# Performance work log

Measured on AMD Instinct MI355X. Metric: run time of the kernel, lower is better.

The kernel has to match this reference:

```python
import jax, jax.numpy as jnp
import numpy as np

B = 256      # graphs per batch
N = 512      # nodes per graph (uniform)
D = 256      # in_channels
DEG = 16     # avg degree for synthetic edges
RATIO = 0.5
K = int(np.ceil(RATIO * N))  # nodes kept per graph = 256


def setup_inputs() -> dict:
    key = jax.random.key(0)
    k1, k2, k3 = jax.random.split(key, 3)
    x = jax.random.normal(k1, (B * N, D), dtype=jnp.float32)
    weight = jax.random.normal(k2, (D,), dtype=jnp.float32)  # TopKPooling score weight
    edge_index = jax.random.randint(k3, (2, B * N * DEG), 0, B * N, dtype=jnp.int64)
    batch = jnp.repeat(jnp.arange(B, dtype=jnp.int64), N)  # graph id per node
    return {"x": x, "weight": weight, "edge_index": edge_index, "batch": batch}


def reference(x, weight, edge_index, batch):
    # PyG TopKPooling: score = tanh((x . w) / ||w||); keep per-graph top-k nodes;
    # pooled features = x[perm] * score[perm]; then global_mean_pool over each graph.
    # Edge filtering/reindexing in TopKPooling does not affect this module's output
    # (forward returns only the mean-pooled node features), so edge_index/batch are
    # consumed but the filtered edges are dead w.r.t. the returned value.
    del edge_index, batch
    score = jnp.tanh((x @ weight) / jnp.linalg.norm(weight))          # [B*N]
    score_bn = score.reshape(B, N)                                     # segment-wise view
    top_s, top_i = jax.lax.top_k(score_bn, K)                          # [B,K] per-graph topk
    x_bn = x.reshape(B, N, D)
    x_sel = jnp.take_along_axis(x_bn, top_i[:, :, None], axis=1)       # [B,K,D] gather
    pooled = x_sel * top_s[:, :, None]                                 # gate by tanh score
    return pooled.mean(axis=1)                                         # global_mean_pool -> [B,D]
```

## Files before the change

kernel.cpp:

```cpp
#include <hip/hip_runtime.h>
#include <math.h>
#include <stdint.h>

#define BG 256
#define NN 512
#define DD 256
#define KK 256
#define WAVES 16

__device__ __forceinline__ uint32_t flip_f32(float f) {
    const uint32_t u = __float_as_uint(f);
    return (u & 0x80000000u) ? ~u : (u | 0x80000000u);
}

__global__ __launch_bounds__(1024) void topk_pool_fused(const float* __restrict__ x,
                                                        const float* __restrict__ w,
                                                        float* __restrict__ out) {
    __shared__ float s[NN];
    __shared__ int   lidx[KK];
    __shared__ float lval[KK];
    __shared__ float red[WAVES][DD];

    const int b    = blockIdx.x;
    const int wv   = threadIdx.x >> 6;
    const int lane = threadIdx.x & 63;

    const float4 w4 = *reinterpret_cast<const float4*>(w + lane * 4);
    float nw = fmaf(w4.x, w4.x, fmaf(w4.y, w4.y, fmaf(w4.z, w4.z, w4.w * w4.w)));
#pragma unroll
    for (int off = 32; off >= 1; off >>= 1) nw += __shfl_xor(nw, off);
    const float inv_nrm = rsqrtf(nw);

    const float* xg = x + (size_t)b * NN * DD;

    {
        const float* xp = xg + (size_t)(wv * 32) * DD + lane * 4;
#pragma unroll
        for (int r0 = 0; r0 < 32; r0 += 8) {
            float d[8];
#pragma unroll
            for (int j = 0; j < 8; ++j) {
                const float4 a = *reinterpret_cast<const float4*>(xp + (size_t)(r0 + j) * DD);
                d[j] = fmaf(a.x, w4.x, fmaf(a.y, w4.y, fmaf(a.z, w4.z, a.w * w4.w)));
            }
#pragma unroll
            for (int off = 32; off >= 1; off >>= 1) {
#pragma unroll
                for (int j = 0; j < 8; ++j) d[j] += __shfl_xor(d[j], off);
            }
#pragma unroll
            for (int j = 0; j < 8; ++j) d[j] = tanhf(d[j] * inv_nrm);
            if (lane == 0) {
                float4 o0 = {d[0], d[1], d[2], d[3]};
                float4 o1 = {d[4], d[5], d[6], d[7]};
                *reinterpret_cast<float4*>(&s[wv * 32 + r0])     = o0;
                *reinterpret_cast<float4*>(&s[wv * 32 + r0 + 4]) = o1;
            }
        }
    }
    __syncthreads();

    if (wv == 0) {
        float sv[8];
        const float4 a0 = *reinterpret_cast<const float4*>(&s[lane * 8]);
        const float4 a1 = *reinterpret_cast<const float4*>(&s[lane * 8 + 4]);
        sv[0] = a0.x; sv[1] = a0.y; sv[2] = a0.z; sv[3] = a0.w;
        sv[4] = a1.x; sv[5] = a1.y; sv[6] = a1.z; sv[7] = a1.w;

        uint32_t u[8];
#pragma unroll
        for (int j = 0; j < 8; ++j) u[j] = flip_f32(sv[j]);

        uint32_t p = 0u;
        for (int bit = 31; bit >= 0; --bit) {
            const uint32_t cand = p | (1u << bit);
            int cnt = 0;
#pragma unroll
            for (int j = 0; j < 8; ++j)
                cnt += __popcll(__ballot(u[j] >= cand));
            if (cnt >= KK) p = cand;
        }

        unsigned long long bt[8];
        int cgt = 0;
#pragma unroll
        for (int j = 0; j < 8; ++j) {
            cgt += __popcll(__ballot(u[j] > p));
            bt[j] = __ballot(u[j] == p);
        }
        const int need = KK - cgt;
        const unsigned long long below = ((unsigned long long)1 << lane) - 1ull;

        int tie_rank = 0;
#pragma unroll
        for (int j = 0; j < 8; ++j) tie_rank += __popcll(bt[j] & below);

        bool selj[8];
        int ntie = 0;
#pragma unroll
        for (int j = 0; j < 8; ++j) {
            const bool gt  = (u[j] > p);
            const bool tie = (u[j] == p);
            selj[j] = gt || (tie && (tie_rank + ntie) < need);
            ntie += tie ? 1 : 0;
        }

        unsigned long long bs[8];
#pragma unroll
        for (int j = 0; j < 8; ++j) bs[j] = __ballot(selj[j]);
        int slot = 0;
#pragma unroll
        for (int j = 0; j < 8; ++j) slot += __popcll(bs[j] & below);

#pragma unroll
        for (int j = 0; j < 8; ++j) {
            if (selj[j]) {
                lidx[slot] = lane * 8 + j;
                lval[slot] = sv[j] * (1.0f / (float)KK);
                ++slot;
            }
        }
    }
    __syncthreads();

    int   idx[KK / WAVES];
    float svv[KK / WAVES];
#pragma unroll
    for (int r = 0; r < KK / WAVES; ++r) {
        idx[r] = lidx[wv * (KK / WAVES) + r];
        svv[r] = lval[wv * (KK / WAVES) + r];
    }

    float4 acc = {0.f, 0.f, 0.f, 0.f};
#pragma unroll
    for (int r = 0; r < KK / WAVES; ++r) {
        const float4 x4 = *reinterpret_cast<const float4*>(xg + (size_t)idx[r] * DD + lane * 4);
        acc.x = fmaf(svv[r], x4.x, acc.x);
        acc.y = fmaf(svv[r], x4.y, acc.y);
        acc.z = fmaf(svv[r], x4.z, acc.z);
        acc.w = fmaf(svv[r], x4.w, acc.w);
    }
    *reinterpret_cast<float4*>(&red[wv][lane * 4]) = acc;
    __syncthreads();

    if (threadIdx.x < DD) {
        const int t = threadIdx.x;
        float v = 0.f;
#pragma unroll
        for (int wq = 0; wq < WAVES; ++wq) v += red[wq][t];
        out[b * DD + t] = v;
    }
}

extern "C" void kernel_launch(void* const* d_in, const int* in_sizes, int n_in,
                              void* d_out, int out_size, void* d_ws, size_t ws_size,
                              hipStream_t stream) {
    const float* x = (const float*)d_in[0];
    const float* w = (const float*)d_in[1];
    float* out = (float*)d_out;
    (void)d_ws; (void)ws_size;

    topk_pool_fused<<<BG, 1024, 0, stream>>>(x, w, out);
}
```

Baseline: 210.1 us.

## Hold each graph's rows in registers and LDS to skip the gather re-read

Each block now keeps its graph's 512 rows on chip while scoring them: part goes into a large LDS tile and the rest stays in per-thread float4 registers. The pooled sum is then a dense, gated reduction over all rows (unselected rows get weight zero) instead of a second gather from global memory. Every wave runs the radix top-k select redundantly, so there is no single-wave serial phase. Scores are ranked on the raw dot product, and tanh is applied only to selected entries. The costs are very high LDS and register use, which limits each CU to one 8-wave block, and extra FMAs on rows that were not selected.

```diff
diff --git a/kernel.cpp b/kernel.cpp
--- a/kernel.cpp
+++ b/kernel.cpp
@@ -6,19 +6,25 @@
 #define NN 512
 #define DD 256
 #define KK 256
-#define WAVES 16
+#define WAVES 8
+#define ROWS_W (NN / WAVES)
+#define LDSR_W 16
+#define REGR_W (ROWS_W - LDSR_W)
 
 __device__ __forceinline__ uint32_t flip_f32(float f) {
     const uint32_t u = __float_as_uint(f);
     return (u & 0x80000000u) ? ~u : (u | 0x80000000u);
 }
+__device__ __forceinline__ float unflip_f32(uint32_t u) {
+    return __uint_as_float((u & 0x80000000u) ? (u ^ 0x80000000u) : ~u);
+}
 
-__global__ __launch_bounds__(1024) void topk_pool_fused(const float* __restrict__ x,
-                                                        const float* __restrict__ w,
-                                                        float* __restrict__ out) {
+__global__ __launch_bounds__(512, 2) void topk_pool_fused(const float* __restrict__ x,
+                                                          const float* __restrict__ w,
+                                                          float* __restrict__ out) {
+    __shared__ float xs[WAVES * LDSR_W][DD];
     __shared__ float s[NN];
-    __shared__ int   lidx[KK];
-    __shared__ float lval[KK];
+    __shared__ float g[NN];
     __shared__ float red[WAVES][DD];
 
     const int b    = blockIdx.x;
@@ -32,44 +38,67 @@
     const float inv_nrm = rsqrtf(nw);
 
     const float* xg = x + (size_t)b * NN * DD;
+    const int r0 = wv * ROWS_W;
+    const float* xp = xg + (size_t)r0 * DD + lane * 4;
 
-    {
-        const float* xp = xg + (size_t)(wv * 32) * DD + lane * 4;
 #pragma unroll
-        for (int r0 = 0; r0 < 32; r0 += 8) {
-            float d[8];
+    for (int bt = 0; bt < LDSR_W / 8; ++bt) {
+        float4 a[8];
+        float  d[8];
 #pragma unroll
-            for (int j = 0; j < 8; ++j) {
-                const float4 a = *reinterpret_cast<const float4*>(xp + (size_t)(r0 + j) * DD);
-                d[j] = fmaf(a.x, w4.x, fmaf(a.y, w4.y, fmaf(a.z, w4.z, a.w * w4.w)));
-            }
+        for (int j = 0; j < 8; ++j)
+            a[j] = *reinterpret_cast<const float4*>(xp + (size_t)(bt * 8 + j) * DD);
 #pragma unroll
-            for (int off = 32; off >= 1; off >>= 1) {
+        for (int j = 0; j < 8; ++j)
+            d[j] = fmaf(a[j].x, w4.x, fmaf(a[j].y, w4.y, fmaf(a[j].z, w4.z, a[j].w * w4.w)));
 #pragma unroll
-                for (int j = 0; j < 8; ++j) d[j] += __shfl_xor(d[j], off);
-            }
+        for (int off = 32; off >= 1; off >>= 1) {
 #pragma unroll
-            for (int j = 0; j < 8; ++j) d[j] = tanhf(d[j] * inv_nrm);
-            if (lane == 0) {
-                float4 o0 = {d[0], d[1], d[2], d[3]};
-                float4 o1 = {d[4], d[5], d[6], d[7]};
-                *reinterpret_cast<float4*>(&s[wv * 32 + r0])     = o0;
-                *reinterpret_cast<float4*>(&s[wv * 32 + r0 + 4]) = o1;
-            }
+            for (int j = 0; j < 8; ++j) d[j] += __shfl_xor(d[j], off);
+        }
+#pragma unroll
+        for (int j = 0; j < 8; ++j)
+            *reinterpret_cast<float4*>(&xs[wv * LDSR_W + bt * 8 + j][lane * 4]) = a[j];
+        if (lane == 0) {
+            float4 o0 = {d[0], d[1], d[2], d[3]};
+            float4 o1 = {d[4], d[5], d[6], d[7]};
+            *reinterpret_cast<float4*>(&s[r0 + bt * 8])     = o0;
+            *reinterpret_cast<float4*>(&s[r0 + bt * 8 + 4]) = o1;
+        }
+    }
+
+    float4 h[REGR_W];
+#pragma unroll
+    for (int bt = 0; bt < REGR_W / 8; ++bt) {
+        float d[8];
+#pragma unroll
+        for (int j = 0; j < 8; ++j)
+            h[bt * 8 + j] = *reinterpret_cast<const float4*>(xp + (size_t)(LDSR_W + bt * 8 + j) * DD);
+#pragma unroll
+        for (int j = 0; j < 8; ++j) {
+            const float4 a = h[bt * 8 + j];
+            d[j] = fmaf(a.x, w4.x, fmaf(a.y, w4.y, fmaf(a.z, w4.z, a.w * w4.w)));
+        }
+#pragma unroll
+        for (int off = 32; off >= 1; off >>= 1) {
+#pragma unroll
+            for (int j = 0; j < 8; ++j) d[j] += __shfl_xor(d[j], off);
+        }
+        if (lane == 0) {
+            float4 o0 = {d[0], d[1], d[2], d[3]};
+            float4 o1 = {d[4], d[5], d[6], d[7]};
+            *reinterpret_cast<float4*>(&s[r0 + LDSR_W + bt * 8])     = o0;
+            *reinterpret_cast<float4*>(&s[r0 + LDSR_W + bt * 8 + 4]) = o1;
         }
     }
     __syncthreads();
 
-    if (wv == 0) {
-        float sv[8];
+    {
         const float4 a0 = *reinterpret_cast<const float4*>(&s[lane * 8]);
         const float4 a1 = *reinterpret_cast<const float4*>(&s[lane * 8 + 4]);
-        sv[0] = a0.x; sv[1] = a0.y; sv[2] = a0.z; sv[3] = a0.w;
-        sv[4] = a1.x; sv[5] = a1.y; sv[6] = a1.z; sv[7] = a1.w;
-
         uint32_t u[8];
-#pragma unroll
-        for (int j = 0; j < 8; ++j) u[j] = flip_f32(sv[j]);
+        u[0] = flip_f32(a0.x); u[1] = flip_f32(a0.y); u[2] = flip_f32(a0.z); u[3] = flip_f32(a0.w);
+        u[4] = flip_f32(a1.x); u[5] = flip_f32(a1.y); u[6] = flip_f32(a1.z); u[7] = flip_f32(a1.w);
 
         uint32_t p = 0u;
         for (int bit = 31; bit >= 0; --bit) {
@@ -81,64 +110,55 @@
             if (cnt >= KK) p = cand;
         }
 
-        unsigned long long bt[8];
+        unsigned long long bt8[8];
         int cgt = 0;
 #pragma unroll
         for (int j = 0; j < 8; ++j) {
             cgt += __popcll(__ballot(u[j] > p));
-            bt[j] = __ballot(u[j] == p);
+            bt8[j] = __ballot(u[j] == p);
         }
         const int need = KK - cgt;
         const unsigned long long below = ((unsigned long long)1 << lane) - 1ull;
 
         int tie_rank = 0;
 #pragma unroll
-        for (int j = 0; j < 8; ++j) tie_rank += __popcll(bt[j] & below);
+        for (int j = 0; j < 8; ++j) tie_rank += __popcll(bt8[j] & below);
 
-        bool selj[8];
+        float gv[8];
         int ntie = 0;
 #pragma unroll
         for (int j = 0; j < 8; ++j) {
-            const bool gt  = (u[j] > p);
             const bool tie = (u[j] == p);
-            selj[j] = gt || (tie && (tie_rank + ntie) < need);
+            const bool sel = (u[j] > p) || (tie && (tie_rank + ntie) < need);
+            gv[j] = sel ? tanhf(unflip_f32(u[j]) * inv_nrm) * (1.0f / (float)KK) : 0.0f;
             ntie += tie ? 1 : 0;
         }
 
-        unsigned long long bs[8];
-#pragma unroll
-        for (int j = 0; j < 8; ++j) bs[j] = __ballot(selj[j]);
-        int slot = 0;
-#pragma unroll
-        for (int j = 0; j < 8; ++j) slot += __popcll(bs[j] & below);
-
-#pragma unroll
-        for (int j = 0; j < 8; ++j) {
-            if (selj[j]) {
-                lidx[slot] = lane * 8 + j;
-                lval[slot] = sv[j] * (1.0f / (float)KK);
-                ++slot;
-            }
+        if ((lane >> 3) == wv) {
+            float4 g0 = {gv[0], gv[1], gv[2], gv[3]};
+            float4 g1 = {gv[4], gv[5], gv[6], gv[7]};
+            *reinterpret_cast<float4*>(&g[lane * 8])     = g0;
+            *reinterpret_cast<float4*>(&g[lane * 8 + 4]) = g1;
         }
-    }
-    __syncthreads();
-
-    int   idx[KK / WAVES];
-    float svv[KK / WAVES];
-#pragma unroll
-    for (int r = 0; r < KK / WAVES; ++r) {
-        idx[r] = lidx[wv * (KK / WAVES) + r];
-        svv[r] = lval[wv * (KK / WAVES) + r];
     }
 
     float4 acc = {0.f, 0.f, 0.f, 0.f};
 #pragma unroll
-    for (int r = 0; r < KK / WAVES; ++r) {
-        const float4 x4 = *reinterpret_cast<const float4*>(xg + (size_t)idx[r] * DD + lane * 4);
-        acc.x = fmaf(svv[r], x4.x, acc.x);
-        acc.y = fmaf(svv[r], x4.y, acc.y);
-        acc.z = fmaf(svv[r], x4.z, acc.z);
-        acc.w = fmaf(svv[r], x4.w, acc.w);
+    for (int j = 0; j < LDSR_W; ++j) {
+        const float gj = g[r0 + j];
+        const float4 v = *reinterpret_cast<const float4*>(&xs[wv * LDSR_W + j][lane * 4]);
+        acc.x = fmaf(gj, v.x, acc.x);
+        acc.y = fmaf(gj, v.y, acc.y);
+        acc.z = fmaf(gj, v.z, acc.z);
+        acc.w = fmaf(gj, v.w, acc.w);
+    }
+#pragma unroll
+    for (int q = 0; q < REGR_W; ++q) {
+        const float gq = g[r0 + LDSR_W + q];
+        acc.x = fmaf(gq, h[q].x, acc.x);
+        acc.y = fmaf(gq, h[q].y, acc.y);
+        acc.z = fmaf(gq, h[q].z, acc.z);
+        acc.w = fmaf(gq, h[q].w, acc.w);
     }
     *reinterpret_cast<float4*>(&red[wv][lane * 4]) = acc;
     __syncthreads();
@@ -160,5 +180,5 @@
     float* out = (float*)d_out;
     (void)d_ws; (void)ws_size;
 
-    topk_pool_fused<<<BG, 1024, 0, stream>>>(x, w, out);
+    topk_pool_fused<<<BG, 512, 0, stream>>>(x, w, out);
 }
```

Result: no change. 207.5 us (-1.2%).
